# Optimization experiments

Hardware: AMD Instinct MI355X
Metric: run time of the kernel (lower is better)

## Reference

```python
import jax, jax.numpy as jnp
import numpy as np


def conv2d(x, w, b, pad=1):
    y = jax.lax.conv_general_dilated(x, w, (1, 1), [(pad, pad), (pad, pad)],
                                     dimension_numbers=('NCHW', 'OIHW', 'NCHW'))
    return y + b[None, :, None, None]


def deform_conv2d(x, offsets, w, b, groups=8, pad=1):
    # torchvision-style deformable conv: offsets [B, 2*G*K, H, W] laid out as
    # (g, k, (dy, dx)); input channels split into G offset groups; zero padding
    # outside the image for bilinear sampling.
    B, C, H, W = x.shape
    kh, kw = w.shape[2], w.shape[3]
    K = kh * kw
    cpg = C // groups
    off = offsets.reshape(B, groups, K, 2, H, W)
    dy, dx = off[:, :, :, 0], off[:, :, :, 1]  # [B,G,K,H,W]
    ky, kx = jnp.meshgrid(jnp.arange(kh), jnp.arange(kw), indexing='ij')
    ky = ky.reshape(K).astype(x.dtype)
    kx = kx.reshape(K).astype(x.dtype)
    ygrid = jnp.arange(H, dtype=x.dtype)
    xgrid = jnp.arange(W, dtype=x.dtype)
    # absolute sampling positions [B,G,K,H,W]
    py = ygrid[None, None, None, :, None] + (ky - pad)[None, None, :, None, None] + dy
    px = xgrid[None, None, None, None, :] + (kx - pad)[None, None, :, None, None] + dx
    y0 = jnp.floor(py)
    x0 = jnp.floor(px)
    wy = py - y0  # frac weights [B,G,K,H,W]
    wx = px - x0
    y0i = y0.astype(jnp.int32)
    x0i = x0.astype(jnp.int32)
    xg = x.reshape(B, groups, cpg, H * W)

    def gather(yc, xc):
        valid = ((yc >= 0) & (yc < H) & (xc >= 0) & (xc < W)).astype(x.dtype)
        idx = jnp.clip(yc, 0, H - 1) * W + jnp.clip(xc, 0, W - 1)
        idx = jnp.broadcast_to(idx.reshape(B, groups, 1, K * H * W),
                               (B, groups, cpg, K * H * W))
        v = jnp.take_along_axis(xg, idx, axis=3).reshape(B, groups, cpg, K, H, W)
        return v * valid[:, :, None]

    v00 = gather(y0i, x0i)
    v01 = gather(y0i, x0i + 1)
    v10 = gather(y0i + 1, x0i)
    v11 = gather(y0i + 1, x0i + 1)
    wy_ = wy[:, :, None]  # [B,G,1,K,H,W]
    wx_ = wx[:, :, None]
    sampled = (v00 * (1 - wy_) * (1 - wx_) + v01 * (1 - wy_) * wx_
               + v10 * wy_ * (1 - wx_) + v11 * wy_ * wx_)
    sampled = sampled.reshape(B, C, K, H, W)
    out = jnp.einsum('bckhw,ock->bohw', sampled, w.reshape(w.shape[0], C, K))
    return out + b[None, :, None, None]


def dab(feat, aux_in, aux_w, aux_b, fw1, fb1, fw2, fb2, se_w1, se_b1, se_w2, se_b2):
    # Adaptive fusion block: project aux (128->64), concat, conv-relu-conv body,
    # SE channel attention (reduction=2), residual add onto feat.
    aux = jax.nn.relu(conv2d(aux_in, aux_w, aux_b))
    x = jnp.concatenate([feat, aux], axis=1)  # [B,128,H,W]
    x = jax.nn.relu(conv2d(x, fw1, fb1))      # 128->64
    x = conv2d(x, fw2, fb2)                   # 64->64
    g = jnp.mean(x, axis=(2, 3))              # [B,64]
    a = jax.nn.sigmoid(jax.nn.relu(g @ se_w1.T + se_b1) @ se_w2.T + se_b2)
    return feat + x * a[:, :, None, None]


def setup_inputs() -> dict:
    key = jax.random.key(0)
    ks = jax.random.split(key, 16)
    B, H, W = 4, 192, 192

    def p(k, shape, s=0.05):
        return jax.random.normal(k, shape, jnp.float32) * s

    return {
        'mv': jax.random.normal(ks[0], (B, 128, H, W), jnp.float32),
        'ref_feature': jax.random.normal(ks[1], (B, 64, H, W), jnp.float32),
        'head_w': p(ks[2], (144, 128, 3, 3)), 'head_b': jnp.zeros((144,), jnp.float32),
        'dcn_w': p(ks[3], (64, 64, 3, 3)), 'dcn_b': jnp.zeros((64,), jnp.float32),
        'c1w1': p(ks[4], (128, 64, 3, 3)), 'c1b1': jnp.zeros((128,), jnp.float32),
        'c1w2': p(ks[5], (128, 128, 3, 3)), 'c1b2': jnp.zeros((128,), jnp.float32),
        'aux_w': p(ks[6], (64, 128, 3, 3)), 'aux_b': jnp.zeros((64,), jnp.float32),
        'fw1': p(ks[7], (64, 128, 3, 3)), 'fb1': jnp.zeros((64,), jnp.float32),
        'fw2': p(ks[8], (64, 64, 3, 3)), 'fb2': jnp.zeros((64,), jnp.float32),
        'se_w1': p(ks[9], (32, 64)), 'se_b1': jnp.zeros((32,), jnp.float32),
        'se_w2': p(ks[10], (64, 32)), 'se_b2': jnp.zeros((64,), jnp.float32),
    }


def reference(mv, ref_feature, head_w, head_b, dcn_w, dcn_b, c1w1, c1b1, c1w2, c1b2,
              aux_w, aux_b, fw1, fb1, fw2, fb2, se_w1, se_b1, se_w2, se_b2):
    offsets = conv2d(mv, head_w, head_b)                       # [B,144,H,W]
    def_feat = jax.nn.relu(deform_conv2d(ref_feature, offsets, dcn_w, dcn_b))
    aux_in = jax.nn.relu(conv2d(jax.nn.relu(conv2d(ref_feature, c1w1, c1b1)),
                                c1w2, c1b2))                   # convs1: 64->128->128
    return dab(def_feat, aux_in, aux_w, aux_b, fw1, fb1, fw2, fb2,
               se_w1, se_b1, se_w2, se_b2)
```

## Files before the change

### kernel.cpp

```cpp
#include <hip/hip_runtime.h>
#include <math.h>

#define HH 192
#define WW 192
#define HWSZ (HH*WW)
#define BB 4

typedef __attribute__((ext_vector_type(8))) short bf16x8;
typedef __attribute__((ext_vector_type(4))) float f32x4;

__device__ __forceinline__ unsigned short f2bf(float f) {
    unsigned int u = __float_as_uint(f);
    u = (u + 0x7FFFu + ((u >> 16) & 1u)) >> 16;
    return (unsigned short)u;
}
__device__ __forceinline__ float bf2f(unsigned short s) {
    return __uint_as_float(((unsigned int)s) << 16);
}

__global__ void wprep_kernel(const float* __restrict__ w, unsigned short* __restrict__ wb,
                             int cout, int cin)
{
    int idx = blockIdx.x * 256 + threadIdx.x;
    int n = cout * cin * 9;
    if (idx >= n) return;
    int o = idx / (cin * 9);
    int rem = idx - o * cin * 9;
    int c = rem / 9;
    int t = rem - c * 9;
    int nch = cin >> 5;
    wb[((t * nch + (c >> 5)) * cout + o) * 32 + (c & 31)] = f2bf(w[idx]);
}

__global__ void wdef_prep_kernel(const float* __restrict__ w, unsigned short* __restrict__ wb)
{
    int i = blockIdx.x * 256 + threadIdx.x;
    if (i >= 64 * 576) return;
    int o = i / 576, rem = i % 576;
    int c = rem / 9, k = rem - c * 9;
    int K = k * 64 + c;
    wb[((size_t)((K >> 5) * 64 + o)) * 32 + (K & 31)] = f2bf(w[i]);
}

template<int NCH>
__global__ __launch_bounds__(256) void nchw_to_cl32(
    const float* __restrict__ in, unsigned short* __restrict__ outb)
{
    __shared__ float tile[32][68];
    const int tid = threadIdx.x;
    const int bz = blockIdx.z;
    const int b = bz / NCH, ch = bz % NCH;
    const int y = blockIdx.y;
    const int x0 = blockIdx.x * 64;
#pragma unroll
    for (int it = 0; it < 2; ++it) {
        int u = tid + it * 256;
        int c = u >> 4, q = u & 15;
        float4 v = *(const float4*)(in + (((size_t)(b * NCH + ch) * 32 + c) * HH + y) * WW + x0 + q * 4);
        *(float4*)&tile[c][q * 4] = v;
    }
    __syncthreads();
    const int pxl = tid >> 2, c8 = tid & 3;
    bf16x8 ov;
#pragma unroll
    for (int j = 0; j < 8; ++j) ov[j] = (short)f2bf(tile[c8 * 8 + j][pxl]);
    *(bf16x8*)(outb + (((size_t)bz * HH + y) * WW + x0 + pxl) * 32 + c8 * 8) = ov;
}

template<int CIN, int COUT_TILE, bool RELU, int EPI>
__global__ __launch_bounds__(256, 2) void conv3x3_v6(
    const unsigned short* __restrict__ in, const unsigned short* __restrict__ wb,
    const float* __restrict__ bias, void* __restrict__ outp,
    int cTot, int ocBase, int nOc, int coutFull, int nPerXcd)
{
    constexpr int NCH = CIN / 32;
    constexpr int NOC = COUT_TILE / 16;
    __shared__ __align__(16) unsigned short sx[6 * 72 * 32];

    const int tid = threadIdx.x;
    const int d = blockIdx.x;
    const int w = (d & 7) * nPerXcd + (d >> 3);
    const int ocT = (w % nOc) * COUT_TILE;
    int t = w / nOc;
    const int x0 = (t % 3) * 64; t /= 3;
    const int y0 = (t % 48) * 4;
    const int b  = t / 48;
    const int wv = tid >> 6, lane = tid & 63;
    const int l15 = lane & 15, kg = lane >> 4;

    f32x4 acc[NOC][4];
#pragma unroll
    for (int oc = 0; oc < NOC; ++oc)
#pragma unroll
        for (int s = 0; s < 4; ++s) acc[oc][s] = (f32x4){0.f, 0.f, 0.f, 0.f};

    for (int ch = 0; ch < NCH; ++ch) {
#pragma unroll
        for (int it = 0; it < 7; ++it) {
            int u = tid + it * 256;
            if (u < 1728) {
                int r = u / 288;
                int rem = u - r * 288;
                int px = rem >> 2, c8 = rem & 3;
                int yin = y0 - 1 + r;
                int gx  = x0 - 4 + px;
                bf16x8 v = {0,0,0,0,0,0,0,0};
                if (yin >= 0 && yin < HH && gx >= 0 && gx < WW)
                    v = *(const bf16x8*)(in + (((size_t)(b * NCH + ch) * HH + yin) * WW + gx) * 32 + c8 * 8);
                *(bf16x8*)&sx[(r * 72 + px) * 32 + ((c8 ^ ((px >> 1) & 3)) << 3)] = v;
            }
        }
        __syncthreads();
#pragma unroll
        for (int ky = 0; ky < 3; ++ky) {
#pragma unroll
            for (int kx = 0; kx < 3; ++kx) {
                const int r = wv + ky;
                bf16x8 bf[4];
#pragma unroll
                for (int s = 0; s < 4; ++s) {
                    int p = s * 16 + l15 + kx + 3;
                    bf[s] = *(const bf16x8*)&sx[(r * 72 + p) * 32 + ((kg ^ ((p >> 1) & 3)) << 3)];
                }
                const unsigned short* wp = wb
                    + ((size_t)(((ky * 3 + kx) * NCH + ch) * coutFull) + ocT + l15) * 32 + kg * 8;
#pragma unroll
                for (int oc = 0; oc < NOC; ++oc) {
                    bf16x8 a = *(const bf16x8*)(wp + oc * 16 * 32);
#pragma unroll
                    for (int s = 0; s < 4; ++s)
                        acc[oc][s] = __builtin_amdgcn_mfma_f32_16x16x32_bf16(a, bf[s], acc[oc][s], 0, 0, 0);
                }
            }
        }
        __syncthreads();
    }
    const int y = y0 + wv;
    if (EPI == 1) {
        float* out = (float*)outp;
#pragma unroll
        for (int oc = 0; oc < NOC; ++oc)
#pragma unroll
            for (int s = 0; s < 4; ++s) {
                int xo = x0 + s * 16 + l15;
#pragma unroll
                for (int j = 0; j < 4; ++j) {
                    int oL = ocT + oc * 16 + kg * 4 + j;
                    float rv = acc[oc][s][j] + bias[oL];
                    if (RELU) rv = fmaxf(rv, 0.f);
                    out[((size_t)(b * cTot + ocBase + oL) * HH + y) * WW + xo] = rv;
                }
            }
    } else if (EPI == 2) {
        unsigned short* out = (unsigned short*)outp;
#pragma unroll
        for (int oc = 0; oc < NOC; ++oc)
#pragma unroll
            for (int s = 0; s < 4; ++s) {
                int xo = x0 + s * 16 + l15;
#pragma unroll
                for (int j = 0; j < 4; ++j) {
                    int oL = ocT + oc * 16 + kg * 4 + j;
                    float rv = acc[oc][s][j] + bias[oL];
                    if (RELU) rv = fmaxf(rv, 0.f);
                    out[((size_t)(b * cTot + ocBase + oL) * HH + y) * WW + xo] = f2bf(rv);
                }
            }
    } else {
        unsigned short* out = (unsigned short*)outp;
#pragma unroll
        for (int oc = 0; oc < NOC; ++oc) {
            int oL = ocT + oc * 16 + kg * 4;
            int o0 = ocBase + oL;
#pragma unroll
            for (int s = 0; s < 4; ++s) {
                int xo = x0 + s * 16 + l15;
                ushort4 u;
                float r0 = acc[oc][s][0] + bias[oL + 0];
                float r1 = acc[oc][s][1] + bias[oL + 1];
                float r2 = acc[oc][s][2] + bias[oL + 2];
                float r3 = acc[oc][s][3] + bias[oL + 3];
                if (RELU) { r0 = fmaxf(r0,0.f); r1 = fmaxf(r1,0.f); r2 = fmaxf(r2,0.f); r3 = fmaxf(r3,0.f); }
                u.x = f2bf(r0); u.y = f2bf(r1); u.z = f2bf(r2); u.w = f2bf(r3);
                *(ushort4*)(out + ((((size_t)(b * cTot + (o0 >> 5)) * HH + y) * WW + xo) * 32) + (o0 & 31)) = u;
            }
        }
    }
}

__global__ __launch_bounds__(512, 2) void deform_v5(
    const unsigned short* __restrict__ xb, const unsigned short* __restrict__ offb,
    const unsigned short* __restrict__ wdefb2, const float* __restrict__ bias,
    unsigned short* __restrict__ cat)
{
    __shared__ __align__(16) unsigned short smp[64 * 584];
    const int tid = threadIdx.x;
    const int b = blockIdx.z;
    int flat = blockIdx.x;
    int nf = (flat & 7) * 72 + (flat >> 3);
    const int pixbase = nf * 64;

    const int px = tid & 63, g = tid >> 6;
    const int pix = pixbase + px;
    const int y = pix / WW, x = pix - y * WW;

    const char* xgb = (const char*)(xb + ((size_t)(b * 2 + (g >> 2)) * HWSZ) * 32 + (g & 3) * 8);
    const unsigned short* ob = offb + ((size_t)(b * 144 + g * 18)) * HWSZ + pix;

    int   voff_[9][4];
    float wv_[9][4];
#pragma unroll
    for (int k = 0; k < 9; ++k) {
        float dy = bf2f(ob[(size_t)(2 * k) * HWSZ]);
        float dx = bf2f(ob[(size_t)(2 * k + 1) * HWSZ]);
        float pyf = (float)(y + k / 3 - 1) + dy;
        float pxf = (float)(x + k % 3 - 1) + dx;
        float fy = floorf(pyf), fx = floorf(pxf);
        float wy = pyf - fy, wx = pxf - fx;
        int iy = (int)fy, ix = (int)fx;
        float w00 = (1.f - wy) * (1.f - wx), w01 = (1.f - wy) * wx;
        float w10 = wy * (1.f - wx),         w11 = wy * wx;
        bool y0v = (iy >= 0) && (iy < HH);
        bool y1v = (iy + 1 >= 0) && (iy + 1 < HH);
        bool x0v = (ix >= 0) && (ix < WW);
        bool x1v = (ix + 1 >= 0) && (ix + 1 < WW);
        if (!(y0v && x0v)) w00 = 0.f;
        if (!(y0v && x1v)) w01 = 0.f;
        if (!(y1v && x0v)) w10 = 0.f;
        if (!(y1v && x1v)) w11 = 0.f;
        int cy0 = min(max(iy, 0), HH - 1), cy1 = min(max(iy + 1, 0), HH - 1);
        int cx0 = min(max(ix, 0), WW - 1), cx1 = min(max(ix + 1, 0), WW - 1);
        voff_[k][0] = (cy0 * WW + cx0) * 64;
        voff_[k][1] = (cy0 * WW + cx1) * 64;
        voff_[k][2] = (cy1 * WW + cx0) * 64;
        voff_[k][3] = (cy1 * WW + cx1) * 64;
        wv_[k][0] = w00; wv_[k][1] = w01; wv_[k][2] = w10; wv_[k][3] = w11;
    }
    unsigned short* so = smp + px * 584 + g * 8;
    bf16x8 cur0 = *(const bf16x8*)(xgb + voff_[0][0]);
    bf16x8 cur1 = *(const bf16x8*)(xgb + voff_[0][1]);
    bf16x8 cur2 = *(const bf16x8*)(xgb + voff_[0][2]);
    bf16x8 cur3 = *(const bf16x8*)(xgb + voff_[0][3]);
#pragma unroll
    for (int k = 0; k < 9; ++k) {
        bf16x8 n0, n1, n2, n3;
        if (k < 8) {
            n0 = *(const bf16x8*)(xgb + voff_[k + 1][0]);
            n1 = *(const bf16x8*)(xgb + voff_[k + 1][1]);
            n2 = *(const bf16x8*)(xgb + voff_[k + 1][2]);
            n3 = *(const bf16x8*)(xgb + voff_[k + 1][3]);
        }
        bf16x8 ov;
#pragma unroll
        for (int cc = 0; cc < 8; ++cc) {
            float s = bf2f((unsigned short)cur0[cc]) * wv_[k][0]
                    + bf2f((unsigned short)cur1[cc]) * wv_[k][1]
                    + bf2f((unsigned short)cur2[cc]) * wv_[k][2]
                    + bf2f((unsigned short)cur3[cc]) * wv_[k][3];
            ov[cc] = (short)f2bf(s);
        }
        *(bf16x8*)(so + k * 64) = ov;
        if (k < 8) { cur0 = n0; cur1 = n1; cur2 = n2; cur3 = n3; }
    }
    __syncthreads();
    const int wv = tid >> 6;
    const int lane = tid & 63, l15 = lane & 15, kg = lane >> 4;
    const int oc = wv >> 1, sp = (wv & 1) * 2;
    f32x4 acc0 = (f32x4){0.f, 0.f, 0.f, 0.f};
    f32x4 acc1 = (f32x4){0.f, 0.f, 0.f, 0.f};
    const unsigned short* arow = wdefb2 + ((size_t)(oc * 16 + l15)) * 32 + kg * 8;
#pragma unroll
    for (int ch = 0; ch < 18; ++ch) {
        bf16x8 b0 = *(const bf16x8*)&smp[(sp * 16 + l15) * 584 + ch * 32 + kg * 8];
        bf16x8 b1 = *(const bf16x8*)&smp[((sp + 1) * 16 + l15) * 584 + ch * 32 + kg * 8];
        bf16x8 a = *(const bf16x8*)(arow + (size_t)ch * 64 * 32);
        acc0 = __builtin_amdgcn_mfma_f32_16x16x32_bf16(a, b0, acc0, 0, 0, 0);
        acc1 = __builtin_amdgcn_mfma_f32_16x16x32_bf16(a, b1, acc1, 0, 0, 0);
    }
    const int o0 = oc * 16 + kg * 4;
#pragma unroll
    for (int s = 0; s < 2; ++s) {
        const f32x4& av = s ? acc1 : acc0;
        int pxo = pixbase + (sp + s) * 16 + l15;
        int yo = pxo / WW, xo = pxo - yo * WW;
        ushort4 u;
        u.x = f2bf(fmaxf(av[0] + bias[o0 + 0], 0.f));
        u.y = f2bf(fmaxf(av[1] + bias[o0 + 1], 0.f));
        u.z = f2bf(fmaxf(av[2] + bias[o0 + 2], 0.f));
        u.w = f2bf(fmaxf(av[3] + bias[o0 + 3], 0.f));
        *(ushort4*)(cat + ((((size_t)(b * 4 + (o0 >> 5)) * HH + yo) * WW + xo) * 32) + (o0 & 31)) = u;
    }
}

__global__ __launch_bounds__(256) void pool_kernel(const float* __restrict__ x, float* __restrict__ gout)
{
    int bc = blockIdx.x;
    const float* p = x + (size_t)bc * HWSZ;
    int tid = threadIdx.x;
    float s = 0.f;
    for (int i = tid * 4; i < HWSZ; i += 256 * 4) {
        float4 v = *reinterpret_cast<const float4*>(p + i);
        s += v.x + v.y + v.z + v.w;
    }
#pragma unroll
    for (int o = 32; o > 0; o >>= 1) s += __shfl_down(s, o, 64);
    __shared__ float red[4];
    if ((tid & 63) == 0) red[tid >> 6] = s;
    __syncthreads();
    if (tid == 0) gout[bc] = (red[0] + red[1] + red[2] + red[3]) * (1.f / (float)HWSZ);
}

__global__ __launch_bounds__(256) void se_kernel(
    const float* __restrict__ g, const float* __restrict__ w1, const float* __restrict__ b1,
    const float* __restrict__ w2, const float* __restrict__ b2, float* __restrict__ a)
{
    __shared__ float sg[BB * 64];
    __shared__ float sh[BB * 32];
    int tid = threadIdx.x;
    sg[tid] = g[tid];
    __syncthreads();
    if (tid < BB * 32) {
        int b = tid / 32, h = tid % 32;
        float s = b1[h];
        for (int c = 0; c < 64; ++c) s += sg[b * 64 + c] * w1[h * 64 + c];
        sh[b * 32 + h] = fmaxf(s, 0.f);
    }
    __syncthreads();
    {
        int b = tid / 64, o = tid % 64;
        float s = b2[o];
        for (int h = 0; h < 32; ++h) s += sh[b * 32 + h] * w2[o * 32 + h];
        a[tid] = 1.f / (1.f + expf(-s));
    }
}

__global__ __launch_bounds__(256) void final_v2(
    float* __restrict__ out, const unsigned short* __restrict__ catb, const float* __restrict__ a)
{
    const int VPC = HWSZ / 4;
    int v = blockIdx.x * 256 + threadIdx.x;
    int bc = v / VPC, within = v - bc * VPC;
    int b = bc >> 6, c = bc & 63;
    float av = a[bc];
    int pix = within * 4;
    int y = pix / WW, x = pix - y * WW;
    const unsigned short* dbase = catb
        + (((size_t)(b * 4 + (c >> 5)) * HH + y) * WW + x) * 32 + (c & 31);
    float4 xo = reinterpret_cast<float4*>(out)[v];
    float4 r;
    r.x = bf2f(dbase[0])  + xo.x * av;
    r.y = bf2f(dbase[32]) + xo.y * av;
    r.z = bf2f(dbase[64]) + xo.z * av;
    r.w = bf2f(dbase[96]) + xo.w * av;
    reinterpret_cast<float4*>(out)[v] = r;
}

extern "C" void kernel_launch(void* const* d_in, const int* in_sizes, int n_in,
                              void* d_out, int out_size, void* d_ws, size_t ws_size,
                              hipStream_t stream) {
    const float* mv     = (const float*)d_in[0];
    const float* ref    = (const float*)d_in[1];
    const float* head_w = (const float*)d_in[2];
    const float* head_b = (const float*)d_in[3];
    const float* dcn_w  = (const float*)d_in[4];
    const float* dcn_b  = (const float*)d_in[5];
    const float* c1w1   = (const float*)d_in[6];
    const float* c1b1   = (const float*)d_in[7];
    const float* c1w2   = (const float*)d_in[8];
    const float* c1b2   = (const float*)d_in[9];
    const float* aux_w  = (const float*)d_in[10];
    const float* aux_b  = (const float*)d_in[11];
    const float* fw1    = (const float*)d_in[12];
    const float* fb1    = (const float*)d_in[13];
    const float* fw2    = (const float*)d_in[14];
    const float* fb2    = (const float*)d_in[15];
    const float* se_w1  = (const float*)d_in[16];
    const float* se_b1  = (const float*)d_in[17];
    const float* se_w2  = (const float*)d_in[18];
    const float* se_b2  = (const float*)d_in[19];
    float* out = (float*)d_out;

    float* ws = (float*)d_ws;
    unsigned short* offb     = (unsigned short*)ws;
    unsigned short* mvb      = (unsigned short*)(ws + 21233664);
    unsigned short* refb     = (unsigned short*)(ws + 30670848);
    unsigned short* catb     = (unsigned short*)(ws + 35389440);
    unsigned short* r2b      = (unsigned short*)(ws + 44826624);
    unsigned short* wdefb2   = (unsigned short*)(ws + 54263808);
    unsigned short* wbb      = (unsigned short*)(ws + 54282240);
    float* gbuf              = ws + 54567936;
    float* abuf              = gbuf + 256;
    unsigned short* t1b      = (unsigned short*)ws;

    unsigned short* wb_head = wbb;
    unsigned short* wb_c1w1 = wb_head + 165888;
    unsigned short* wb_c1w2 = wb_c1w1 + 73728;
    unsigned short* wb_aux  = wb_c1w2 + 147456;
    unsigned short* wb_fw1  = wb_aux  + 73728;
    unsigned short* wb_fw2  = wb_fw1  + 73728;

    wdef_prep_kernel<<<144, 256, 0, stream>>>(dcn_w, wdefb2);
    wprep_kernel<<<(144*128*9 + 255)/256, 256, 0, stream>>>(head_w, wb_head, 144, 128);
    wprep_kernel<<<(128*64*9  + 255)/256, 256, 0, stream>>>(c1w1,   wb_c1w1, 128, 64);
    wprep_kernel<<<(128*128*9 + 255)/256, 256, 0, stream>>>(c1w2,   wb_c1w2, 128, 128);
    wprep_kernel<<<(64*128*9  + 255)/256, 256, 0, stream>>>(aux_w,  wb_aux,  64, 128);
    wprep_kernel<<<(64*128*9  + 255)/256, 256, 0, stream>>>(fw1,    wb_fw1,  64, 128);
    wprep_kernel<<<(64*64*9   + 255)/256, 256, 0, stream>>>(fw2,    wb_fw2,  64, 64);

    nchw_to_cl32<4><<<dim3(3, 192, BB * 4), 256, 0, stream>>>(mv,  mvb);
    nchw_to_cl32<2><<<dim3(3, 192, BB * 2), 256, 0, stream>>>(ref, refb);

    conv3x3_v6<128, 48, false, 2><<<1728, 256, 0, stream>>>(
        mvb, wb_head, head_b, offb, 144, 0, 3, 144, 216);
    deform_v5<<<dim3(576, 1, BB), 512, 0, stream>>>(refb, offb, wdefb2, dcn_b, catb);
    conv3x3_v6<64, 64, true, 0><<<1152, 256, 0, stream>>>(
        refb, wb_c1w1, c1b1, t1b, 4, 0, 2, 128, 144);
    conv3x3_v6<128, 64, true, 0><<<1152, 256, 0, stream>>>(
        t1b, wb_c1w2, c1b2, r2b, 4, 0, 2, 128, 144);
    conv3x3_v6<128, 32, true, 0><<<1152, 256, 0, stream>>>(
        r2b, wb_aux, aux_b, catb, 4, 64, 2, 64, 144);
    conv3x3_v6<128, 32, true, 0><<<1152, 256, 0, stream>>>(
        catb, wb_fw1, fb1, r2b, 2, 0, 2, 64, 144);
    conv3x3_v6<64, 32, false, 1><<<1152, 256, 0, stream>>>(
        r2b, wb_fw2, fb2, out, 64, 0, 2, 64, 144);
    pool_kernel<<<BB * 64, 256, 0, stream>>>(out, gbuf);
    se_kernel<<<1, 256, 0, stream>>>(gbuf, se_w1, se_b1, se_w2, se_b2, abuf);
    final_v2<<<9216, 256, 0, stream>>>(out, catb, abuf);
}
```

Before: 505.3 us.

## Merge prep/transpose launches, raise occupancy bounds, deepen deform gather prefetch

Folds the seven weight-prep launches into one kernel and the two NCHW-to-channel-last transposes into one, removing per-launch overhead. Raises the launch_bounds min-blocks hint on the conv kernels to 3 and on the deformable kernel to 4, which pushes the compiler to use fewer registers. Restructures the deformable sampler to compute bilinear offsets lazily, two taps ahead, with a schedule barrier, instead of precomputing all nine taps. Lower register budgets risk spills in the MFMA conv kernels.

Result: faster. 490.4 us (-2.9%).

```diff
diff --git a/kernel.cpp b/kernel.cpp
--- a/kernel.cpp
+++ b/kernel.cpp
@@ -18,12 +18,31 @@
     return __uint_as_float(((unsigned int)s) << 16);
 }
 
-__global__ void wprep_kernel(const float* __restrict__ w, unsigned short* __restrict__ wb,
-                             int cout, int cin)
+__global__ void prep_all(
+    const float* __restrict__ head_w, const float* __restrict__ c1w1,
+    const float* __restrict__ c1w2,   const float* __restrict__ aux_w,
+    const float* __restrict__ fw1,    const float* __restrict__ fw2,
+    const float* __restrict__ dcn_w,
+    unsigned short* __restrict__ wb_head, unsigned short* __restrict__ wb_c1w1,
+    unsigned short* __restrict__ wb_c1w2, unsigned short* __restrict__ wb_aux,
+    unsigned short* __restrict__ wb_fw1,  unsigned short* __restrict__ wb_fw2,
+    unsigned short* __restrict__ wdefb2)
 {
     int idx = blockIdx.x * 256 + threadIdx.x;
-    int n = cout * cin * 9;
-    if (idx >= n) return;
+    const float* w; unsigned short* wb; int cout, cin;
+    if (idx < 165888)                 { w = head_w; wb = wb_head; cout = 144; cin = 128; }
+    else if ((idx -= 165888) < 73728) { w = c1w1;   wb = wb_c1w1; cout = 128; cin = 64;  }
+    else if ((idx -= 73728) < 147456) { w = c1w2;   wb = wb_c1w2; cout = 128; cin = 128; }
+    else if ((idx -= 147456) < 73728) { w = aux_w;  wb = wb_aux;  cout = 64;  cin = 128; }
+    else if ((idx -= 73728) < 73728)  { w = fw1;    wb = wb_fw1;  cout = 64;  cin = 128; }
+    else if ((idx -= 73728) < 36864)  { w = fw2;    wb = wb_fw2;  cout = 64;  cin = 64;  }
+    else if ((idx -= 36864) < 36864) {
+        int o = idx / 576, rem = idx % 576;
+        int c = rem / 9, k = rem - c * 9;
+        int K = k * 64 + c;
+        wdefb2[((size_t)((K >> 5) * 64 + o)) * 32 + (K & 31)] = f2bf(dcn_w[idx]);
+        return;
+    } else return;
     int o = idx / (cin * 9);
     int rem = idx - o * cin * 9;
     int c = rem / 9;
@@ -32,31 +51,23 @@
     wb[((t * nch + (c >> 5)) * cout + o) * 32 + (c & 31)] = f2bf(w[idx]);
 }
 
-__global__ void wdef_prep_kernel(const float* __restrict__ w, unsigned short* __restrict__ wb)
-{
-    int i = blockIdx.x * 256 + threadIdx.x;
-    if (i >= 64 * 576) return;
-    int o = i / 576, rem = i % 576;
-    int c = rem / 9, k = rem - c * 9;
-    int K = k * 64 + c;
-    wb[((size_t)((K >> 5) * 64 + o)) * 32 + (K & 31)] = f2bf(w[i]);
-}
-
-template<int NCH>
-__global__ __launch_bounds__(256) void nchw_to_cl32(
-    const float* __restrict__ in, unsigned short* __restrict__ outb)
+__global__ __launch_bounds__(256) void transpose_all(
+    const float* __restrict__ mv, const float* __restrict__ ref,
+    unsigned short* __restrict__ mvb, unsigned short* __restrict__ refb)
 {
     __shared__ float tile[32][68];
     const int tid = threadIdx.x;
-    const int bz = blockIdx.z;
-    const int b = bz / NCH, ch = bz % NCH;
+    int bz = blockIdx.z;
+    const float* in; unsigned short* outb;
+    if (bz < 16) { in = mv;  outb = mvb;  }
+    else         { in = ref; outb = refb; bz -= 16; }
     const int y = blockIdx.y;
     const int x0 = blockIdx.x * 64;
 #pragma unroll
     for (int it = 0; it < 2; ++it) {
         int u = tid + it * 256;
         int c = u >> 4, q = u & 15;
-        float4 v = *(const float4*)(in + (((size_t)(b * NCH + ch) * 32 + c) * HH + y) * WW + x0 + q * 4);
+        float4 v = *(const float4*)(in + (((size_t)bz * 32 + c) * HH + y) * WW + x0 + q * 4);
         *(float4*)&tile[c][q * 4] = v;
     }
     __syncthreads();
@@ -68,7 +79,7 @@
 }
 
 template<int CIN, int COUT_TILE, bool RELU, int EPI>
-__global__ __launch_bounds__(256, 2) void conv3x3_v6(
+__global__ __launch_bounds__(256, 3) void conv3x3_v7(
     const unsigned short* __restrict__ in, const unsigned short* __restrict__ wb,
     const float* __restrict__ bias, void* __restrict__ outp,
     int cTot, int ocBase, int nOc, int coutFull, int nPerXcd)
@@ -188,7 +199,7 @@
     }
 }
 
-__global__ __launch_bounds__(512, 2) void deform_v5(
+__global__ __launch_bounds__(512, 4) void deform_v6(
     const unsigned short* __restrict__ xb, const unsigned short* __restrict__ offb,
     const unsigned short* __restrict__ wdefb2, const float* __restrict__ bias,
     unsigned short* __restrict__ cat)
@@ -207,14 +218,16 @@
     const char* xgb = (const char*)(xb + ((size_t)(b * 2 + (g >> 2)) * HWSZ) * 32 + (g & 3) * 8);
     const unsigned short* ob = offb + ((size_t)(b * 144 + g * 18)) * HWSZ + pix;
 
-    int   voff_[9][4];
-    float wv_[9][4];
+    float dyv[9], dxv[9];
 #pragma unroll
     for (int k = 0; k < 9; ++k) {
-        float dy = bf2f(ob[(size_t)(2 * k) * HWSZ]);
-        float dx = bf2f(ob[(size_t)(2 * k + 1) * HWSZ]);
-        float pyf = (float)(y + k / 3 - 1) + dy;
-        float pxf = (float)(x + k % 3 - 1) + dx;
+        dyv[k] = bf2f(ob[(size_t)(2 * k) * HWSZ]);
+        dxv[k] = bf2f(ob[(size_t)(2 * k + 1) * HWSZ]);
+    }
+
+    auto calc = [&](int k, int vo[4], float w4[4]) {
+        float pyf = (float)(y + k / 3 - 1) + dyv[k];
+        float pxf = (float)(x + k % 3 - 1) + dxv[k];
         float fy = floorf(pyf), fx = floorf(pxf);
         float wy = pyf - fy, wx = pxf - fx;
         int iy = (int)fy, ix = (int)fx;
@@ -230,37 +243,48 @@
         if (!(y1v && x1v)) w11 = 0.f;
         int cy0 = min(max(iy, 0), HH - 1), cy1 = min(max(iy + 1, 0), HH - 1);
         int cx0 = min(max(ix, 0), WW - 1), cx1 = min(max(ix + 1, 0), WW - 1);
-        voff_[k][0] = (cy0 * WW + cx0) * 64;
-        voff_[k][1] = (cy0 * WW + cx1) * 64;
-        voff_[k][2] = (cy1 * WW + cx0) * 64;
-        voff_[k][3] = (cy1 * WW + cx1) * 64;
-        wv_[k][0] = w00; wv_[k][1] = w01; wv_[k][2] = w10; wv_[k][3] = w11;
+        vo[0] = (cy0 * WW + cx0) * 64;
+        vo[1] = (cy0 * WW + cx1) * 64;
+        vo[2] = (cy1 * WW + cx0) * 64;
+        vo[3] = (cy1 * WW + cx1) * 64;
+        w4[0] = w00; w4[1] = w01; w4[2] = w10; w4[3] = w11;
+    };
+
+    float wr[3][4];
+    bf16x8 pf[2][4];
+    {
+        int vo[4]; calc(0, vo, wr[0]);
+#pragma unroll
+        for (int j = 0; j < 4; ++j) pf[0][j] = *(const bf16x8*)(xgb + vo[j]);
+    }
+    {
+        int vo[4]; calc(1, vo, wr[1]);
+#pragma unroll
+        for (int j = 0; j < 4; ++j) pf[1][j] = *(const bf16x8*)(xgb + vo[j]);
     }
     unsigned short* so = smp + px * 584 + g * 8;
-    bf16x8 cur0 = *(const bf16x8*)(xgb + voff_[0][0]);
-    bf16x8 cur1 = *(const bf16x8*)(xgb + voff_[0][1]);
-    bf16x8 cur2 = *(const bf16x8*)(xgb + voff_[0][2]);
-    bf16x8 cur3 = *(const bf16x8*)(xgb + voff_[0][3]);
 #pragma unroll
     for (int k = 0; k < 9; ++k) {
-        bf16x8 n0, n1, n2, n3;
-        if (k < 8) {
-            n0 = *(const bf16x8*)(xgb + voff_[k + 1][0]);
-            n1 = *(const bf16x8*)(xgb + voff_[k + 1][1]);
-            n2 = *(const bf16x8*)(xgb + voff_[k + 1][2]);
-            n3 = *(const bf16x8*)(xgb + voff_[k + 1][3]);
+        bf16x8 nx0, nx1, nx2, nx3;
+        if (k + 2 < 9) {
+            int vo[4]; calc(k + 2, vo, wr[(k + 2) % 3]);
+            nx0 = *(const bf16x8*)(xgb + vo[0]);
+            nx1 = *(const bf16x8*)(xgb + vo[1]);
+            nx2 = *(const bf16x8*)(xgb + vo[2]);
+            nx3 = *(const bf16x8*)(xgb + vo[3]);
         }
+        __builtin_amdgcn_sched_barrier(0);
         bf16x8 ov;
 #pragma unroll
         for (int cc = 0; cc < 8; ++cc) {
-            float s = bf2f((unsigned short)cur0[cc]) * wv_[k][0]
-                    + bf2f((unsigned short)cur1[cc]) * wv_[k][1]
-                    + bf2f((unsigned short)cur2[cc]) * wv_[k][2]
-                    + bf2f((unsigned short)cur3[cc]) * wv_[k][3];
+            float s = bf2f((unsigned short)pf[k & 1][0][cc]) * wr[k % 3][0]
+                    + bf2f((unsigned short)pf[k & 1][1][cc]) * wr[k % 3][1]
+                    + bf2f((unsigned short)pf[k & 1][2][cc]) * wr[k % 3][2]
+                    + bf2f((unsigned short)pf[k & 1][3][cc]) * wr[k % 3][3];
             ov[cc] = (short)f2bf(s);
         }
         *(bf16x8*)(so + k * 64) = ov;
-        if (k < 8) { cur0 = n0; cur1 = n1; cur2 = n2; cur3 = n3; }
+        if (k + 2 < 9) { pf[k & 1][0] = nx0; pf[k & 1][1] = nx1; pf[k & 1][2] = nx2; pf[k & 1][3] = nx3; }
     }
     __syncthreads();
     const int wv = tid >> 6;
@@ -399,29 +423,22 @@
     unsigned short* wb_fw1  = wb_aux  + 73728;
     unsigned short* wb_fw2  = wb_fw1  + 73728;
 
-    wdef_prep_kernel<<<144, 256, 0, stream>>>(dcn_w, wdefb2);
-    wprep_kernel<<<(144*128*9 + 255)/256, 256, 0, stream>>>(head_w, wb_head, 144, 128);
-    wprep_kernel<<<(128*64*9  + 255)/256, 256, 0, stream>>>(c1w1,   wb_c1w1, 128, 64);
-    wprep_kernel<<<(128*128*9 + 255)/256, 256, 0, stream>>>(c1w2,   wb_c1w2, 128, 128);
-    wprep_kernel<<<(64*128*9  + 255)/256, 256, 0, stream>>>(aux_w,  wb_aux,  64, 128);
-    wprep_kernel<<<(64*128*9  + 255)/256, 256, 0, stream>>>(fw1,    wb_fw1,  64, 128);
-    wprep_kernel<<<(64*64*9   + 255)/256, 256, 0, stream>>>(fw2,    wb_fw2,  64, 64);
-
-    nchw_to_cl32<4><<<dim3(3, 192, BB * 4), 256, 0, stream>>>(mv,  mvb);
-    nchw_to_cl32<2><<<dim3(3, 192, BB * 2), 256, 0, stream>>>(ref, refb);
-
-    conv3x3_v6<128, 48, false, 2><<<1728, 256, 0, stream>>>(
+    prep_all<<<2376, 256, 0, stream>>>(head_w, c1w1, c1w2, aux_w, fw1, fw2, dcn_w,
+                                       wb_head, wb_c1w1, wb_c1w2, wb_aux, wb_fw1, wb_fw2, wdefb2);
+    transpose_all<<<dim3(3, 192, 24), 256, 0, stream>>>(mv, ref, mvb, refb);
+
+    conv3x3_v7<128, 48, false, 2><<<1728, 256, 0, stream>>>(
         mvb, wb_head, head_b, offb, 144, 0, 3, 144, 216);
-    deform_v5<<<dim3(576, 1, BB), 512, 0, stream>>>(refb, offb, wdefb2, dcn_b, catb);
-    conv3x3_v6<64, 64, true, 0><<<1152, 256, 0, stream>>>(
+    deform_v6<<<dim3(576, 1, BB), 512, 0, stream>>>(refb, offb, wdefb2, dcn_b, catb);
+    conv3x3_v7<64, 64, true, 0><<<1152, 256, 0, stream>>>(
         refb, wb_c1w1, c1b1, t1b, 4, 0, 2, 128, 144);
-    conv3x3_v6<128, 64, true, 0><<<1152, 256, 0, stream>>>(
+    conv3x3_v7<128, 64, true, 0><<<1152, 256, 0, stream>>>(
         t1b, wb_c1w2, c1b2, r2b, 4, 0, 2, 128, 144);
-    conv3x3_v6<128, 32, true, 0><<<1152, 256, 0, stream>>>(
+    conv3x3_v7<128, 32, true, 0><<<1152, 256, 0, stream>>>(
         r2b, wb_aux, aux_b, catb, 4, 64, 2, 64, 144);
-    conv3x3_v6<128, 32, true, 0><<<1152, 256, 0, stream>>>(
+    conv3x3_v7<128, 32, true, 0><<<1152, 256, 0, stream>>>(
         catb, wb_fw1, fb1, r2b, 2, 0, 2, 64, 144);
-    conv3x3_v6<64, 32, false, 1><<<1152, 256, 0, stream>>>(
+    conv3x3_v7<64, 32, false, 1><<<1152, 256, 0, stream>>>(
         r2b, wb_fw2, fb2, out, 64, 0, 2, 64, 144);
     pool_kernel<<<BB * 64, 256, 0, stream>>>(out, gbuf);
     se_kernel<<<1, 256, 0, stream>>>(gbuf, se_w1, se_b1, se_w2, se_b2, abuf);
```
